# Kernel optimization log

Hardware: AMD Instinct MI355X
Metric: run time of the kernel (lower is better)

## Reference

```python
import jax, jax.numpy as jnp
import numpy as np

H = 16          # num_heads
D = 4           # att_size (hard-coded in module)
HID = 256       # hidden_size
B, N = 4, 1024
SCALE = D ** (-0.5)
BN_EPS = 1e-5
NEG_SLOPE = 0.2


def setup_inputs() -> dict:
    key = jax.random.key(0)
    ks = jax.random.split(key, 12)
    s = 0.05
    return {
        "q": jax.random.normal(ks[0], (B, HID, N), jnp.float32),
        "k": jax.random.normal(ks[1], (B, HID, N), jnp.float32),
        "v": jax.random.normal(ks[2], (B, HID, N), jnp.float32),
        "attn_bias": jax.random.normal(ks[3], (B, H, N, N), jnp.float32),
        # 1x1 Conv1d weights (kernel dim squeezed): [out_ch, in_ch]
        "Wq": jax.random.normal(ks[4], (H * D, HID), jnp.float32) * s,
        "Wk": jax.random.normal(ks[5], (H * D, HID), jnp.float32) * s,
        "Wv": jax.random.normal(ks[6], (H * D, HID), jnp.float32) * s,
        "Wo": jax.random.normal(ks[7], (HID, H * D), jnp.float32) * s,
        "bo": jax.random.normal(ks[8], (HID,), jnp.float32) * s,
        "gamma": jnp.ones((HID,), jnp.float32),
        "beta": jnp.zeros((HID,), jnp.float32),
        "run_mean": jnp.zeros((HID,), jnp.float32),
        "run_var": jnp.ones((HID,), jnp.float32),
    }


def reference(q, k, v, attn_bias, Wq, Wk, Wv, Wo, bo, gamma, beta, run_mean, run_var):
    # 1x1 conv projections: [B, HID, N] -> [B, H*D, N]
    qp = jnp.einsum('oc,bcn->bon', Wq, q)
    kp = jnp.einsum('oc,bcn->bon', Wk, k)
    vp = jnp.einsum('oc,bcn->bon', Wv, v)
    # faithful (non-standard) view: [B, H*D, N] -> [B, D, N, H]
    qh = qp.reshape(B, D, N, H).transpose(0, 3, 2, 1)   # [B, H, N, D]
    vh = vp.reshape(B, D, N, H).transpose(0, 3, 2, 1)   # [B, H, N, D]
    kh = kp.reshape(B, D, N, H).transpose(0, 3, 1, 2)   # [B, H, D, N]
    # scaled dot-product attention with additive bias
    scores = jnp.einsum('bhnd,bhdm->bhnm', qh, kh) * SCALE + attn_bias
    attn = jax.nn.softmax(scores, axis=-1)              # dropout rate 0.0 (eval)
    x = jnp.einsum('bhnm,bhmd->bhnd', attn, vh)         # [B, H, N, D]
    # transpose(3,2) then view(B, H*D, N)
    x = x.transpose(0, 1, 3, 2).reshape(B, H * D, N)
    # output 1x1 conv + BatchNorm1d (eval, running stats) + LeakyReLU(0.2)
    y = jnp.einsum('oc,bcn->bon', Wo, x) + bo[None, :, None]
    inv = jax.lax.rsqrt(run_var + BN_EPS)
    y = (y - run_mean[None, :, None]) * (gamma * inv)[None, :, None] + beta[None, :, None]
    return jnp.where(y > 0, y, NEG_SLOPE * y)
```

## Files before the change

### kernel.cpp

```cpp
#include <hip/hip_runtime.h>

#define HID 256
#define NSEQ 1024
#define NH 16
#define DH 4
#define NB 4
#define SCALEF 0.5f
#define HEADSZ (NB * NH * NSEQ * DH)

typedef float f4 __attribute__((ext_vector_type(4)));

__device__ __forceinline__ float rfl(float x) {
    return __builtin_bit_cast(float,
        __builtin_amdgcn_readfirstlane(__builtin_bit_cast(int, x)));
}

__global__ __launch_bounds__(256) void proj_kernel(
    const float* __restrict__ q, const float* __restrict__ k,
    const float* __restrict__ v, const float* __restrict__ Wq,
    const float* __restrict__ Wk, const float* __restrict__ Wv,
    float* __restrict__ ws)
{
    const int tid   = threadIdx.x;
    const int pos_l = tid & 63;
    int cb = __builtin_amdgcn_readfirstlane(tid >> 6);
    const int p    = blockIdx.y;
    const int b    = blockIdx.z;
    const int pos0 = blockIdx.x * 64;

    const float* in = (p == 0) ? q : (p == 1) ? k : v;
    const float* W  = (p == 0) ? Wq : (p == 1) ? Wk : Wv;
    float* dst = ws + (size_t)p * HEADSZ;

    __shared__ float lds_in[64][64];

    const int row_l = tid >> 4;
    const int col4  = tid & 15;
    const float* inb = in + (size_t)b * HID * NSEQ + pos0;

    float acc[16];
#pragma unroll
    for (int j = 0; j < 16; ++j) acc[j] = 0.f;

    f4 vbuf[4];
#pragma unroll
    for (int t = 0; t < 4; ++t)
        vbuf[t] = *(const f4*)(inb + (size_t)(row_l + 16 * t) * NSEQ + col4 * 4);

    for (int c = 0; c < 4; ++c) {
#pragma unroll
        for (int t = 0; t < 4; ++t)
            *(f4*)&lds_in[row_l + 16 * t][col4 * 4] = vbuf[t];
        __syncthreads();
        if (c < 3) {
#pragma unroll
            for (int t = 0; t < 4; ++t)
                vbuf[t] = *(const f4*)(inb +
                    (size_t)((c + 1) * 64 + row_l + 16 * t) * NSEQ + col4 * 4);
        }
#pragma unroll
        for (int i8 = 0; i8 < 64; i8 += 8) {
            float x[8];
#pragma unroll
            for (int j = 0; j < 8; ++j) x[j] = lds_in[i8 + j][pos_l];
#pragma unroll
            for (int kk = 0; kk < 16; ++kk) {
                const float* wr = W + (cb * 16 + kk) * HID + c * 64 + i8;
#pragma unroll
                for (int j = 0; j < 8; ++j)
                    acc[kk] = fmaf(wr[j], x[j], acc[kk]);
            }
        }
        __syncthreads();
    }

    const int pos_g = pos0 + pos_l;
    const int h     = pos_g & 15;
    const int nsub  = pos_g >> 4;
#pragma unroll
    for (int kk = 0; kk < 16; ++kk) {
        int c = cb * 16 + kk;
        int d = c >> 4;
        int n = (c & 15) * 64 + nsub;
        dst[(((size_t)b * NH + h) * NSEQ + n) * DH + d] = acc[kk];
    }
}

__global__ __launch_bounds__(256, 4) void attn_kernel(
    const float* __restrict__ bias, const float* __restrict__ ws,
    float* __restrict__ x2)
{
    const int tid  = threadIdx.x;
    const int lane = tid & 63;
    const int wave = tid >> 6;
    const int h    = blockIdx.y;
    const int b    = blockIdx.z;
    const int n0   = blockIdx.x * 32 + wave * 8;

    const float4* Qh = (const float4*)(ws);
    const float4* Kh = (const float4*)(ws + (size_t)1 * HEADSZ);
    const float4* Vh = (const float4*)(ws + (size_t)2 * HEADSZ);
    const int headbase = (b * NH + h) * NSEQ;
    const int mb = lane * 4;

#define LOG2E 1.44269504f
#define EOFF  (-16.f * LOG2E)

    float qx[8], qy[8], qz[8], qw[8];
#pragma unroll
    for (int r = 0; r < 8; ++r) {
        float4 t = Qh[headbase + n0 + r];
        qx[r] = rfl(t.x); qy[r] = rfl(t.y); qz[r] = rfl(t.z); qw[r] = rfl(t.w);
    }

    float sum[8];
    float o[8][4];
#pragma unroll
    for (int r = 0; r < 8; ++r) {
        sum[r] = 0.f;
        o[r][0] = o[r][1] = o[r][2] = o[r][3] = 0.f;
    }

    const float* bwave = bias + ((size_t)headbase + n0) * NSEQ + mb;

#pragma unroll 1
    for (int c = 0; c < 4; ++c) {
        const int kv = headbase + c * 256 + mb;
        float4 kb[4], vb[4];
#pragma unroll
        for (int i = 0; i < 4; ++i) {
            kb[i] = Kh[kv + i];
            vb[i] = Vh[kv + i];
        }
#pragma unroll
        for (int r = 0; r < 8; ++r) {
            f4 bb = __builtin_nontemporal_load(
                (const f4*)(bwave + (size_t)r * NSEQ + c * 256));
#pragma unroll
            for (int i = 0; i < 4; ++i) {
                float dot = qx[r] * kb[i].x + qy[r] * kb[i].y +
                            qz[r] * kb[i].z + qw[r] * kb[i].w;
                float s = fmaf(dot, SCALEF, bb[i]);
                float e = exp2f(fmaf(s, LOG2E, EOFF));
                sum[r] += e;
                o[r][0] = fmaf(e, vb[i].x, o[r][0]);
                o[r][1] = fmaf(e, vb[i].y, o[r][1]);
                o[r][2] = fmaf(e, vb[i].z, o[r][2]);
                o[r][3] = fmaf(e, vb[i].w, o[r][3]);
            }
        }
    }

#pragma unroll
    for (int r = 0; r < 8; ++r) {
        float s = sum[r], a0 = o[r][0], a1 = o[r][1], a2 = o[r][2], a3 = o[r][3];
#pragma unroll
        for (int st = 1; st < 64; st <<= 1) {
            s  += __shfl_xor(s,  st, 64);
            a0 += __shfl_xor(a0, st, 64);
            a1 += __shfl_xor(a1, st, 64);
            a2 += __shfl_xor(a2, st, 64);
            a3 += __shfl_xor(a3, st, 64);
        }
        float val = (lane == 0) ? a0 : (lane == 1) ? a1 : (lane == 2) ? a2 : a3;
        if (lane < 4)
            x2[((size_t)b * (NH * DH) + h * DH + lane) * NSEQ + n0 + r] = val / s;
    }
}

__global__ __launch_bounds__(256) void out_kernel(
    const float* __restrict__ x2, const float* __restrict__ Wo,
    const float* __restrict__ bo, const float* __restrict__ gamma,
    const float* __restrict__ beta, const float* __restrict__ rmean,
    const float* __restrict__ rvar, float* __restrict__ out)
{
    const int pos4 = threadIdx.x * 4;
    const int o0   = blockIdx.y * 4;
    const int b    = blockIdx.z;

    const float* xb = x2 + (size_t)b * (NH * DH) * NSEQ;

    f4 acc[4];
#pragma unroll
    for (int j = 0; j < 4; ++j) acc[j] = (f4)(0.f);

#pragma unroll 8
    for (int c = 0; c < NH * DH; ++c) {
        f4 x = *(const f4*)(xb + (size_t)c * NSEQ + pos4);
#pragma unroll
        for (int j = 0; j < 4; ++j)
            acc[j] += Wo[(o0 + j) * (NH * DH) + c] * x;
    }
#pragma unroll
    for (int j = 0; j < 4; ++j) {
        int oc = o0 + j;
        float scale = gamma[oc] * rsqrtf(rvar[oc] + 1e-5f);
        f4 y = (acc[j] + (bo[oc] - rmean[oc])) * scale + beta[oc];
        float* dst = out + ((size_t)b * HID + oc) * NSEQ + pos4;
        f4 res;
#pragma unroll
        for (int d = 0; d < 4; ++d) {
            float yy = y[d];
            res[d] = (yy > 0.f) ? yy : 0.2f * yy;
        }
        *(f4*)dst = res;
    }
}

extern "C" void kernel_launch(void* const* d_in, const int* in_sizes, int n_in,
                              void* d_out, int out_size, void* d_ws, size_t ws_size,
                              hipStream_t stream) {
    const float* q     = (const float*)d_in[0];
    const float* k     = (const float*)d_in[1];
    const float* v     = (const float*)d_in[2];
    const float* bias  = (const float*)d_in[3];
    const float* Wq    = (const float*)d_in[4];
    const float* Wk    = (const float*)d_in[5];
    const float* Wv    = (const float*)d_in[6];
    const float* Wo    = (const float*)d_in[7];
    const float* bo    = (const float*)d_in[8];
    const float* gamma = (const float*)d_in[9];
    const float* beta  = (const float*)d_in[10];
    const float* rmean = (const float*)d_in[11];
    const float* rvar  = (const float*)d_in[12];

    float* ws = (float*)d_ws;
    float* x2 = ws + (size_t)3 * HEADSZ;
    float* out = (float*)d_out;

    proj_kernel<<<dim3(NSEQ / 64, 3, NB), 256, 0, stream>>>(q, k, v, Wq, Wk, Wv, ws);
    attn_kernel<<<dim3(NSEQ / 32, NH, NB), 256, 0, stream>>>(bias, ws, x2);
    out_kernel<<<dim3(1, HID / 4, NB), 256, 0, stream>>>(
        x2, Wo, bo, gamma, beta, rmean, rvar, out);
}
```

Measured before the change: 132.1 us.

## Fuse attention with output projection, BatchNorm and LeakyReLU into one kernel

Attention and the output 1x1 conv plus BatchNorm/LeakyReLU now run in one kernel. Each 512-thread block handles 8 query rows of one batch across all 16 heads, with each wave doing two heads. Per-head results go to LDS and are then projected by Wo directly, so the x2 round trip through global memory and one launch are gone. The bias loads also drop the nontemporal hint. In exchange there are only 512 blocks with serialised heads per wave, and the output stores become 16-byte writes scattered across rows.

```diff
diff --git a/kernel.cpp b/kernel.cpp
--- a/kernel.cpp
+++ b/kernel.cpp
@@ -14,6 +14,9 @@
     return __builtin_bit_cast(float,
         __builtin_amdgcn_readfirstlane(__builtin_bit_cast(int, x)));
 }
+
+#define LOG2E 1.44269504f
+#define EOFF  (-16.f * LOG2E)
 
 __global__ __launch_bounds__(256) void proj_kernel(
     const float* __restrict__ q, const float* __restrict__ k,
@@ -86,124 +89,121 @@
     }
 }
 
-__global__ __launch_bounds__(256, 4) void attn_kernel(
+__global__ __launch_bounds__(512, 4) void attn_out_kernel(
     const float* __restrict__ bias, const float* __restrict__ ws,
-    float* __restrict__ x2)
+    const float* __restrict__ Wo, const float* __restrict__ bo,
+    const float* __restrict__ gamma, const float* __restrict__ beta,
+    const float* __restrict__ rmean, const float* __restrict__ rvar,
+    float* __restrict__ out)
 {
     const int tid  = threadIdx.x;
     const int lane = tid & 63;
     const int wave = tid >> 6;
-    const int h    = blockIdx.y;
-    const int b    = blockIdx.z;
-    const int n0   = blockIdx.x * 32 + wave * 8;
+    const int seg  = blockIdx.x;
+    const int b    = blockIdx.y;
+    const int n0   = seg * 8;
+    const int mb   = lane * 4;
 
     const float4* Qh = (const float4*)(ws);
     const float4* Kh = (const float4*)(ws + (size_t)1 * HEADSZ);
     const float4* Vh = (const float4*)(ws + (size_t)2 * HEADSZ);
-    const int headbase = (b * NH + h) * NSEQ;
-    const int mb = lane * 4;
-
-#define LOG2E 1.44269504f
-#define EOFF  (-16.f * LOG2E)
-
-    float qx[8], qy[8], qz[8], qw[8];
-#pragma unroll
-    for (int r = 0; r < 8; ++r) {
-        float4 t = Qh[headbase + n0 + r];
-        qx[r] = rfl(t.x); qy[r] = rfl(t.y); qz[r] = rfl(t.z); qw[r] = rfl(t.w);
-    }
-
-    float sum[8];
-    float o[8][4];
-#pragma unroll
-    for (int r = 0; r < 8; ++r) {
-        sum[r] = 0.f;
-        o[r][0] = o[r][1] = o[r][2] = o[r][3] = 0.f;
-    }
-
-    const float* bwave = bias + ((size_t)headbase + n0) * NSEQ + mb;
+
+    __shared__ float x2l[64][9];
 
 #pragma unroll 1
-    for (int c = 0; c < 4; ++c) {
-        const int kv = headbase + c * 256 + mb;
-        float4 kb[4], vb[4];
-#pragma unroll
-        for (int i = 0; i < 4; ++i) {
-            kb[i] = Kh[kv + i];
-            vb[i] = Vh[kv + i];
-        }
+    for (int h2 = 0; h2 < 2; ++h2) {
+        const int h = wave * 2 + h2;
+        const int headbase = (b * NH + h) * NSEQ;
+
+        float qx[8], qy[8], qz[8], qw[8];
 #pragma unroll
         for (int r = 0; r < 8; ++r) {
-            f4 bb = __builtin_nontemporal_load(
-                (const f4*)(bwave + (size_t)r * NSEQ + c * 256));
+            float4 t = Qh[headbase + n0 + r];
+            qx[r] = rfl(t.x); qy[r] = rfl(t.y);
+            qz[r] = rfl(t.z); qw[r] = rfl(t.w);
+        }
+
+        float sum[8];
+        float o[8][4];
+#pragma unroll
+        for (int r = 0; r < 8; ++r) {
+            sum[r] = 0.f;
+            o[r][0] = o[r][1] = o[r][2] = o[r][3] = 0.f;
+        }
+
+        const float* bwave = bias + ((size_t)headbase + n0) * NSEQ + mb;
+
+#pragma unroll 1
+        for (int c = 0; c < 4; ++c) {
+            const int kv = headbase + c * 256 + mb;
+            float4 kb[4], vb[4];
 #pragma unroll
             for (int i = 0; i < 4; ++i) {
-                float dot = qx[r] * kb[i].x + qy[r] * kb[i].y +
-                            qz[r] * kb[i].z + qw[r] * kb[i].w;
-                float s = fmaf(dot, SCALEF, bb[i]);
-                float e = exp2f(fmaf(s, LOG2E, EOFF));
-                sum[r] += e;
-                o[r][0] = fmaf(e, vb[i].x, o[r][0]);
-                o[r][1] = fmaf(e, vb[i].y, o[r][1]);
-                o[r][2] = fmaf(e, vb[i].z, o[r][2]);
-                o[r][3] = fmaf(e, vb[i].w, o[r][3]);
-            }
-        }
-    }
-
-#pragma unroll
-    for (int r = 0; r < 8; ++r) {
-        float s = sum[r], a0 = o[r][0], a1 = o[r][1], a2 = o[r][2], a3 = o[r][3];
-#pragma unroll
-        for (int st = 1; st < 64; st <<= 1) {
-            s  += __shfl_xor(s,  st, 64);
-            a0 += __shfl_xor(a0, st, 64);
-            a1 += __shfl_xor(a1, st, 64);
-            a2 += __shfl_xor(a2, st, 64);
-            a3 += __shfl_xor(a3, st, 64);
-        }
-        float val = (lane == 0) ? a0 : (lane == 1) ? a1 : (lane == 2) ? a2 : a3;
-        if (lane < 4)
-            x2[((size_t)b * (NH * DH) + h * DH + lane) * NSEQ + n0 + r] = val / s;
-    }
-}
-
-__global__ __launch_bounds__(256) void out_kernel(
-    const float* __restrict__ x2, const float* __restrict__ Wo,
-    const float* __restrict__ bo, const float* __restrict__ gamma,
-    const float* __restrict__ beta, const float* __restrict__ rmean,
-    const float* __restrict__ rvar, float* __restrict__ out)
-{
-    const int pos4 = threadIdx.x * 4;
-    const int o0   = blockIdx.y * 4;
-    const int b    = blockIdx.z;
-
-    const float* xb = x2 + (size_t)b * (NH * DH) * NSEQ;
-
-    f4 acc[4];
-#pragma unroll
-    for (int j = 0; j < 4; ++j) acc[j] = (f4)(0.f);
-
-#pragma unroll 8
-    for (int c = 0; c < NH * DH; ++c) {
-        f4 x = *(const f4*)(xb + (size_t)c * NSEQ + pos4);
-#pragma unroll
-        for (int j = 0; j < 4; ++j)
-            acc[j] += Wo[(o0 + j) * (NH * DH) + c] * x;
-    }
-#pragma unroll
-    for (int j = 0; j < 4; ++j) {
-        int oc = o0 + j;
+                kb[i] = Kh[kv + i];
+                vb[i] = Vh[kv + i];
+            }
+#pragma unroll
+            for (int r = 0; r < 8; ++r) {
+                f4 bb = *(const f4*)(bwave + (size_t)r * NSEQ + c * 256);
+#pragma unroll
+                for (int i = 0; i < 4; ++i) {
+                    float dot = qx[r] * kb[i].x + qy[r] * kb[i].y +
+                                qz[r] * kb[i].z + qw[r] * kb[i].w;
+                    float s = fmaf(dot, SCALEF, bb[i]);
+                    float e = exp2f(fmaf(s, LOG2E, EOFF));
+                    sum[r] += e;
+                    o[r][0] = fmaf(e, vb[i].x, o[r][0]);
+                    o[r][1] = fmaf(e, vb[i].y, o[r][1]);
+                    o[r][2] = fmaf(e, vb[i].z, o[r][2]);
+                    o[r][3] = fmaf(e, vb[i].w, o[r][3]);
+                }
+            }
+        }
+
+#pragma unroll
+        for (int r = 0; r < 8; ++r) {
+            float s = sum[r], a0 = o[r][0], a1 = o[r][1],
+                  a2 = o[r][2], a3 = o[r][3];
+#pragma unroll
+            for (int st = 1; st < 64; st <<= 1) {
+                s  += __shfl_xor(s,  st, 64);
+                a0 += __shfl_xor(a0, st, 64);
+                a1 += __shfl_xor(a1, st, 64);
+                a2 += __shfl_xor(a2, st, 64);
+                a3 += __shfl_xor(a3, st, 64);
+            }
+            float val = (lane == 0) ? a0 : (lane == 1) ? a1
+                      : (lane == 2) ? a2 : a3;
+            if (lane < 4)
+                x2l[h * DH + lane][r] = val / s;
+        }
+    }
+
+    __syncthreads();
+
+    {
+        const int oc = tid & 255;
+        const int rh = tid >> 8;
+        const float* wr = Wo + oc * (NH * DH);
+
+        f4 acc = (f4)(0.f);
+#pragma unroll
+        for (int c = 0; c < NH * DH; ++c) {
+            float wv = wr[c];
+            acc[0] = fmaf(wv, x2l[c][rh * 4 + 0], acc[0]);
+            acc[1] = fmaf(wv, x2l[c][rh * 4 + 1], acc[1]);
+            acc[2] = fmaf(wv, x2l[c][rh * 4 + 2], acc[2]);
+            acc[3] = fmaf(wv, x2l[c][rh * 4 + 3], acc[3]);
+        }
         float scale = gamma[oc] * rsqrtf(rvar[oc] + 1e-5f);
-        f4 y = (acc[j] + (bo[oc] - rmean[oc])) * scale + beta[oc];
-        float* dst = out + ((size_t)b * HID + oc) * NSEQ + pos4;
+        f4 y = (acc + (bo[oc] - rmean[oc])) * scale + beta[oc];
         f4 res;
 #pragma unroll
         for (int d = 0; d < 4; ++d) {
             float yy = y[d];
             res[d] = (yy > 0.f) ? yy : 0.2f * yy;
         }
-        *(f4*)dst = res;
+        *(f4*)(out + ((size_t)b * HID + oc) * NSEQ + n0 + rh * 4) = res;
     }
 }
 
@@ -224,12 +224,10 @@
     const float* rmean = (const float*)d_in[11];
     const float* rvar  = (const float*)d_in[12];
 
-    float* ws = (float*)d_ws;
-    float* x2 = ws + (size_t)3 * HEADSZ;
+    float* ws  = (float*)d_ws;
     float* out = (float*)d_out;
 
     proj_kernel<<<dim3(NSEQ / 64, 3, NB), 256, 0, stream>>>(q, k, v, Wq, Wk, Wv, ws);
-    attn_kernel<<<dim3(NSEQ / 32, NH, NB), 256, 0, stream>>>(bias, ws, x2);
-    out_kernel<<<dim3(1, HID / 4, NB), 256, 0, stream>>>(
-        x2, Wo, bo, gamma, beta, rmean, rvar, out);
-}
+    attn_out_kernel<<<dim3(NSEQ / 8, NB), 512, 0, stream>>>(
+        bias, ws, Wo, bo, gamma, beta, rmean, rvar, out);
+}
```

New measurement: 121.2 us. 1.09x faster.
